# Optimization experiments

Measured on AMD Instinct MI355X. Metric: run time of the kernel, lower is better.

## Reference

```python
import jax, jax.numpy as jnp
import numpy as np
import math
from jax import lax

D = 256      # d_model = out_channel
NH = 8       # n_heads
DEP = D // NH
DFF = 1024
B = 48       # conv batch == attended axis in this model
CIN = 32
HW = 32
S = 30 * 30  # (HW-2)**2 after 3x3 valid conv
OUT = 1
FMAX = float(np.finfo(np.float32).max)


def _p(k, shp, scale=0.02):
    return jax.random.normal(k, shp, jnp.float32) * scale


def setup_inputs():
    key = jax.random.key(0)
    ks = jax.random.split(key, 34)
    return {
        'X_en': jax.random.normal(ks[0], (B, CIN, HW, HW), jnp.float32),
        'X_de': jax.random.normal(ks[1], (B, CIN, HW, HW), jnp.float32),
        'conv1_w': _p(ks[2], (D, CIN, 3, 3)), 'conv1_b': _p(ks[3], (D,)),
        'conv2_w': _p(ks[4], (D, D, 3, 3)), 'conv2_b': _p(ks[5], (D,)),
        'enc_wq': _p(ks[6], (D, D)), 'enc_wk': _p(ks[7], (D, D)), 'enc_wv': _p(ks[8], (D, D)),
        'enc_rel_w': _p(ks[9], (S, NH, DEP, B)),
        'enc_ffn_w1': _p(ks[10], (DFF, D)), 'enc_ffn_b1': _p(ks[11], (DFF,)),
        'enc_ffn_w2': _p(ks[12], (D, DFF)), 'enc_ffn_b2': _p(ks[13], (D,)),
        'dec_m_wq': _p(ks[14], (D, D)), 'dec_m_wk': _p(ks[15], (D, D)), 'dec_m_wv': _p(ks[16], (D, D)),
        'dec_m_rel_w': _p(ks[17], (S, NH, DEP, B)),
        'dec_m_lin1_w': _p(ks[18], (B, B)), 'dec_m_lin1_b': _p(ks[19], (B,)),
        'dec_m_lin2_w': _p(ks[20], (B, B)), 'dec_m_lin2_b': _p(ks[21], (B,)),
        'dec_c_wq': _p(ks[22], (D, D)), 'dec_c_wk': _p(ks[23], (D, D)), 'dec_c_wv': _p(ks[24], (D, D)),
        'dec_c_rel_w': _p(ks[25], (S, NH, DEP, B)),
        'dec_ffn_w1': _p(ks[26], (DFF, D)), 'dec_ffn_b1': _p(ks[27], (DFF,)),
        'dec_ffn_w2': _p(ks[28], (D, DFF)), 'dec_ffn_b2': _p(ks[29], (D,)),
        'out_w': _p(ks[30], (OUT, D)), 'out_b': _p(ks[31], (OUT,)),
    }


def _ln(x, eps=1e-5):
    m = jnp.mean(x, -1, keepdims=True)
    v = jnp.mean((x - m) ** 2, -1, keepdims=True)
    return (x - m) / jnp.sqrt(v + eps)


def _skew(q, w):
    # Music-Transformer relative-position skew: matmul + pad + reshape + slice
    emd = jnp.einsum('shbd,shdj->shbj', q, w)  # (S,NH,b,b)
    s, h, i, j = emd.shape
    l = i + j - 1
    x = jnp.concatenate([emd, jnp.zeros_like(emd)], -1).reshape(s, h, -1)
    pad = (-x.shape[-1]) % l
    x = jnp.pad(x, ((0, 0), (0, 0), (0, pad)))
    return x.reshape(s, h, -1, l)[:, :, :i, i - 1:]


def _mha(xq, xk, xv, wq, wk, wv, rel_w, lins=None):
    b, sl, d = xq.shape
    # raw view (not transpose): (b,sl,d) -> (sl,b,NH,DEP), then swap to (sl,NH,b,DEP)
    q = (xq @ wq.T).reshape(sl, b, NH, DEP).swapaxes(1, 2)
    k = (xk @ wk.T).reshape(sl, b, NH, DEP).swapaxes(1, 2)
    v = (xv @ wv.T).reshape(sl, b, NH, DEP).swapaxes(1, 2)
    scores = jnp.einsum('shid,shjd->shij', q, k) / math.sqrt(DEP)  # (sl,NH,b,b)
    if lins is not None:  # masked path: per-call linears + causal mask
        l1w, l1b, l2w, l2b = lins
        qk = scores @ l1w.T + l1b
        qk = jnp.swapaxes(qk, 2, 3) @ l2w.T + l2b
        mask = jnp.triu(jnp.full((b, b), -FMAX, jnp.float32), 1)
        bmm = qk + mask
    else:
        bmm = scores  # linear1/linear2 outputs are discarded when mask=False
    attn = jax.nn.softmax(bmm + _skew(q, rel_w), axis=0)  # softmax over dim 0 (S)
    out = jnp.einsum('shij,shjd->shid', attn, v)  # (sl,NH,b,DEP)
    return out.reshape(b, sl, NH * DEP)  # view(a_s[2], a_s[0], -1)


def reference(X_en, X_de, conv1_w, conv1_b, conv2_w, conv2_b, enc_wq, enc_wk, enc_wv, enc_rel_w, enc_ffn_w1, enc_ffn_b1, enc_ffn_w2, enc_ffn_b2, dec_m_wq, dec_m_wk, dec_m_wv, dec_m_rel_w, dec_m_lin1_w, dec_m_lin1_b, dec_m_lin2_w, dec_m_lin2_b, dec_c_wq, dec_c_wk, dec_c_wv, dec_c_rel_w, dec_ffn_w1, dec_ffn_b1, dec_ffn_w2, dec_ffn_b2, out_w, out_b):
    def conv(x, w, b_, pad):
        y = lax.conv_general_dilated(x, w, (1, 1), [(pad, pad), (pad, pad)],
                                     dimension_numbers=('NCHW', 'OIHW', 'NCHW'))
        return y + b_[None, :, None, None]

    def convs(x):
        return conv(conv(x, conv1_w, conv1_b, 0), conv2_w, conv2_b, 1)

    xpe = convs(X_en)
    xpd = convs(X_de)
    b, d, h, w = xpe.shape
    x_en = xpe.reshape(b, h * w, d)  # raw reshape as in torch source
    x_de = xpd.reshape(b, h * w, d)
    # encoder layer
    a = _mha(x_en, x_en, x_en, enc_wq, enc_wk, enc_wv, enc_rel_w)
    o1 = _ln(x_en + a)
    f = jax.nn.relu(o1 @ enc_ffn_w1.T + enc_ffn_b1) @ enc_ffn_w2.T + enc_ffn_b2
    enc_out = _ln(o1 + f)
    # decoder layer
    m = _mha(x_de, x_de, x_de, dec_m_wq, dec_m_wk, dec_m_wv, dec_m_rel_w,
             (dec_m_lin1_w, dec_m_lin1_b, dec_m_lin2_w, dec_m_lin2_b))
    h1 = _ln(x_de + m)
    c = _mha(h1, enc_out, enc_out, dec_c_wq, dec_c_wk, dec_c_wv, dec_c_rel_w)
    h2 = _ln(c + h1)
    f2 = jax.nn.relu(h2 @ dec_ffn_w1.T + dec_ffn_b1) @ dec_ffn_w2.T + dec_ffn_b2
    h3 = _ln(h2 + f2)
    y = h3 @ out_w.T + out_b
    return jax.nn.softmax(y, axis=0)
```

## Files before the change

### kernel.cpp

```cpp
#include <hip/hip_runtime.h>
#include <float.h>

typedef __bf16 bf16;
typedef __attribute__((ext_vector_type(8))) __bf16 bf16x8;
typedef __attribute__((ext_vector_type(4))) __bf16 bf16x4;
typedef __attribute__((ext_vector_type(4))) float f32x4;

__device__ __forceinline__ int imin(int a, int b) { return a < b ? a : b; }

__device__ __forceinline__ void gl2lds(const bf16* g, bf16* l) {
  __builtin_amdgcn_global_load_lds(
      (const __attribute__((address_space(1))) void*)g,
      (__attribute__((address_space(3))) void*)l, 16, 0, 0);
}

__global__ void k_zero(bf16* zp) { zp[threadIdx.x] = (bf16)0.0f; }

struct CastSegs { const float* s[13]; bf16* d[13]; int n[13]; };
__global__ void k_cast_all(CastSegs sg, int total) {
  int i = blockIdx.x * 256 + threadIdx.x;
  if (i >= total) return;
  for (int k = 0; k < 13; ++k) {
    if (i < sg.n[k]) { sg.d[k][i] = (bf16)sg.s[k][i]; return; }
    i -= sg.n[k];
  }
}

__global__ __launch_bounds__(256) void k_prep_rel(const float* __restrict__ rel,
                                                  bf16* __restrict__ RelT) {
  __shared__ float tile[32 * 49];
  const int t = threadIdx.x;
  for (int u = 0; u < 8; ++u) {
    const size_t sh = (size_t)blockIdx.x * 8 + u;
    const float* src = rel + sh * 1536;
    bf16* dst = RelT + sh * 1536;
    __syncthreads();
    for (int i = t; i < 1536; i += 256) {
      int k = i / 48, j = i - k * 48;
      tile[k * 49 + j] = src[i];
    }
    __syncthreads();
    for (int i = t; i < 1536; i += 256) {
      int j = i >> 5, k = i & 31;
      dst[i] = (bf16)tile[k * 49 + j];
    }
  }
}

__global__ void k_prep_lin(const float* __restrict__ l1w, const float* __restrict__ l2w,
                           bf16* __restrict__ L1p, bf16* __restrict__ L2p) {
  for (int i = threadIdx.x; i < 3456; i += 256) {
    int r = i / 72, c = i - r * 72;
    L1p[i] = (c < 48) ? (bf16)l1w[r * 48 + c] : (bf16)0.0f;
    L2p[i] = (c < 48) ? (bf16)l2w[r * 48 + c] : (bf16)0.0f;
  }
}

__global__ void k_prep_x(const float* __restrict__ X, bf16* __restrict__ XR) {
  int idx = blockIdx.x * 256 + threadIdx.x;
  if (idx >= 48 * 1024 * 32) return;
  int b = idx >> 15, r = idx & 32767, pos = r >> 5, ic = r & 31;
  XR[idx] = (bf16)X[((size_t)(b * 32 + ic) << 10) + pos];
}

__global__ void k_pack_conv(const float* __restrict__ w, bf16* __restrict__ dst,
                            int OC, int IC, int total) {
  int idx = blockIdx.x * 256 + threadIdx.x;
  if (idx >= total) return;
  int t = idx / (OC * IC);
  int rem = idx - t * OC * IC;
  int oc = rem / IC, ic = rem - oc * IC;
  dst[idx] = (bf16)w[(size_t)(oc * IC + ic) * 9 + t];
}

__global__ __launch_bounds__(256, 2) void k_gemm128(
    const bf16* __restrict__ A, const bf16* __restrict__ B,
    const float* __restrict__ bias, bf16* __restrict__ C,
    int M, int N, int K, int relu, int ldc, int coff) {
  __shared__ alignas(16) bf16 SM[8192];
  bf16* As = SM;
  bf16* Bs = SM + 4096;
  const int t = threadIdx.x, wave = t >> 6;
  const int lane = t & 63, fr = lane & 15, kq = lane >> 4;
  const int wm = wave & 1, wn = wave >> 1;
  const int m0 = blockIdx.x * 128, n0 = blockIdx.y * 128;
  const int srow = t >> 2, kseg = (t & 3) * 8;
  f32x4 acc[4][4] = {};
  const bf16* gA0 = A + (size_t)imin(m0 + srow, M - 1) * K + kseg;
  const bf16* gA1 = A + (size_t)imin(m0 + 64 + srow, M - 1) * K + kseg;
  const bf16* gB0 = B + (size_t)(n0 + srow) * K + kseg;
  const bf16* gB1 = B + (size_t)(n0 + 64 + srow) * K + kseg;
  bf16* sA0 = As + wave * 512;
  bf16* sA1 = As + 2048 + wave * 512;
  bf16* sB0 = Bs + wave * 512;
  bf16* sB1 = Bs + 2048 + wave * 512;
  for (int k0 = 0; k0 < K; k0 += 32) {
    gl2lds(gA0 + k0, sA0);
    gl2lds(gA1 + k0, sA1);
    gl2lds(gB0 + k0, sB0);
    gl2lds(gB1 + k0, sB1);
    __syncthreads();
    bf16x8 af[4], bw[4];
    for (int mt = 0; mt < 4; ++mt)
      af[mt] = *(const bf16x8*)(As + (wm * 64 + mt * 16 + fr) * 32 + kq * 8);
    for (int nt = 0; nt < 4; ++nt)
      bw[nt] = *(const bf16x8*)(Bs + (wn * 64 + nt * 16 + fr) * 32 + kq * 8);
    for (int mt = 0; mt < 4; ++mt)
      for (int nt = 0; nt < 4; ++nt)
        acc[mt][nt] = __builtin_amdgcn_mfma_f32_16x16x32_bf16(af[mt], bw[nt], acc[mt][nt], 0, 0, 0);
    __syncthreads();
  }
  bf16* Cst = SM;
  for (int half = 0; half < 2; ++half) {
    if (wm == half) {
      for (int mt = 0; mt < 4; ++mt)
        for (int nt = 0; nt < 4; ++nt) {
          int n = n0 + wn * 64 + nt * 16 + fr;
          float bv = bias ? bias[n] : 0.0f;
          for (int r = 0; r < 4; ++r) {
            float v = acc[mt][nt][r] + bv;
            if (relu) v = fmaxf(v, 0.0f);
            Cst[(mt * 16 + kq * 4 + r) * 128 + wn * 64 + nt * 16 + fr] = (bf16)v;
          }
        }
    }
    __syncthreads();
    for (int i = t; i < 1024; i += 256) {
      int r = i >> 4, cs = i & 15;
      int gm = m0 + half * 64 + r;
      if (gm < M)
        *(bf16x8*)(C + (size_t)gm * ldc + coff + n0 + cs * 8) = *(const bf16x8*)(Cst + r * 128 + cs * 8);
    }
    __syncthreads();
  }
}

template <int CIN, int PAD, int SRCW, int SRCROWS, int CHECK, int TRANS>
__global__ __launch_bounds__(256, 2) void k_conv128(
    const bf16* __restrict__ A, const bf16* __restrict__ Bp,
    const float* __restrict__ bias, bf16* __restrict__ C,
    const bf16* __restrict__ zpage) {
  __shared__ alignas(16) bf16 SM[8192];
  bf16* As = SM;
  bf16* Bs = SM + 4096;
  const int t = threadIdx.x, wave = t >> 6;
  const int lane = t & 63, fr = lane & 15, kq = lane >> 4;
  const int wm = wave & 1, wn = wave >> 1;
  const int m0 = blockIdx.x * 128, n0 = blockIdx.y * 128;
  const int srow = t >> 2, kseg = (t & 3) * 8;
  f32x4 acc[4][4] = {};
  int bb[2], yy[2], xx[2];
  for (int hf = 0; hf < 2; ++hf) {
    int m = imin(m0 + hf * 64 + srow, 43199);
    int b = m / 900, p = m - b * 900;
    bb[hf] = b; yy[hf] = p / 30; xx[hf] = p - (p / 30) * 30;
  }
  bf16* sA0 = As + wave * 512;
  bf16* sA1 = As + 2048 + wave * 512;
  bf16* sB0 = Bs + wave * 512;
  bf16* sB1 = Bs + 2048 + wave * 512;
  for (int k0 = 0; k0 < CIN; k0 += 32) {
    for (int t9 = 0; t9 < 9; ++t9) {
      const int ky = t9 / 3, kx = t9 - ky * 3;
      const bf16* ga[2];
      for (int hf = 0; hf < 2; ++hf) {
        int sy = yy[hf] + ky - PAD, sx = xx[hf] + kx - PAD;
        bool valid = !CHECK || (sy >= 0 && sy < SRCW && sx >= 0 && sx < SRCW);
        ga[hf] = (valid ? A + (size_t)(bb[hf] * SRCROWS + sy * SRCW + sx) * CIN : zpage) + kseg;
      }
      const bf16* gb = Bp + (size_t)(t9 * 256 + n0 + srow) * CIN + kseg;
      gl2lds(ga[0] + k0, sA0);
      gl2lds(ga[1] + k0, sA1);
      gl2lds(gb + k0, sB0);
      gl2lds(gb + (size_t)64 * CIN + k0, sB1);
      __syncthreads();
      bf16x8 af[4], bw[4];
      for (int mt = 0; mt < 4; ++mt)
        af[mt] = *(const bf16x8*)(As + (wm * 64 + mt * 16 + fr) * 32 + kq * 8);
      for (int nt = 0; nt < 4; ++nt)
        bw[nt] = *(const bf16x8*)(Bs + (wn * 64 + nt * 16 + fr) * 32 + kq * 8);
      for (int mt = 0; mt < 4; ++mt)
        for (int nt = 0; nt < 4; ++nt)
          acc[mt][nt] = __builtin_amdgcn_mfma_f32_16x16x32_bf16(af[mt], bw[nt], acc[mt][nt], 0, 0, 0);
      __syncthreads();
    }
  }
  bf16* Cst = SM;
  for (int half = 0; half < 2; ++half) {
    if (wm == half) {
      for (int mt = 0; mt < 4; ++mt)
        for (int nt = 0; nt < 4; ++nt) {
          int n = n0 + wn * 64 + nt * 16 + fr;
          float bv = bias[n];
          for (int r = 0; r < 4; ++r) {
            float v = acc[mt][nt][r] + bv;
            if (TRANS)
              Cst[(wn * 64 + nt * 16 + fr) * 64 + mt * 16 + kq * 4 + r] = (bf16)v;
            else
              Cst[(mt * 16 + kq * 4 + r) * 128 + wn * 64 + nt * 16 + fr] = (bf16)v;
          }
        }
    }
    __syncthreads();
    if (TRANS) {
      for (int i = t; i < 2048; i += 256) {
        int oc = i >> 4, pc = i & 15;
        int gm = m0 + half * 64 + pc * 4;
        if (gm < 43200) {
          int b = gm / 900, p = gm - b * 900;
          *(bf16x4*)(C + (size_t)(b * 256 + n0 + oc) * 900 + p) = *(const bf16x4*)(Cst + oc * 64 + pc * 4);
        }
      }
    } else {
      for (int i = t; i < 1024; i += 256) {
        int r = i >> 4, cs = i & 15;
        int gm = m0 + half * 64 + r;
        if (gm < 43200)
          *(bf16x8*)(C + (size_t)gm * 256 + n0 + cs * 8) = *(const bf16x8*)(Cst + r * 128 + cs * 8);
      }
    }
    __syncthreads();
  }
}

template <int MASKED>
__global__ __launch_bounds__(256, MASKED ? 4 : 5) void k_attn_z(
    const bf16* __restrict__ QKV, const bf16* __restrict__ RelT, bf16* __restrict__ Z,
    const bf16* __restrict__ L1p, const bf16* __restrict__ L2p,
    const float* __restrict__ l1b, const float* __restrict__ l2b) {
  __shared__ alignas(16) bf16 QKs[2][48 * 40];
  __shared__ float EMD[48 * 49];
  __shared__ alignas(16) bf16 zst[48 * 48];
  __shared__ alignas(16) bf16 Sc[MASKED ? 48 * 72 : 8];
  __shared__ alignas(16) bf16 T2b[MASKED ? 48 * 72 : 8];
  const int sh = blockIdx.x, s = sh >> 3, h = sh & 7;
  const int t = threadIdx.x, wave = t >> 6, lane = t & 63, fr = lane & 15, kq = lane >> 4;
  const float scale = 0.17677669529663687f;
  for (int c = t; c < 384; c += 256) {
    int half = c >= 192 ? 1 : 0, cc = c - half * 192;
    int row = cc >> 2, seg = cc & 3;
    *(bf16x8*)(&QKs[half][row * 40 + seg * 8]) =
        *(const bf16x8*)(QKV + (size_t)(s * 48 + row) * 768 + half * 256 + h * 32 + seg * 8);
  }
  if constexpr (MASKED) {
    for (int i = t; i < 768; i += 256) {
      int r = i >> 4, c = 48 + (i & 15);
      Sc[r * 72 + c] = (bf16)0.0f;
      T2b[r * 72 + c] = (bf16)0.0f;
    }
  }
  __syncthreads();
  const bf16* relb = RelT + (size_t)sh * 1536;
  f32x4 sreg[3];
  int u = 0;
  for (int t9 = wave; t9 < 9; t9 += 4, ++u) {
    int ti = t9 / 3, tj = t9 - ti * 3;
    bf16x8 af = *(const bf16x8*)(&QKs[0][(ti * 16 + fr) * 40 + kq * 8]);
    bf16x8 bk = *(const bf16x8*)(&QKs[1][(tj * 16 + fr) * 40 + kq * 8]);
    bf16x8 rf = *(const bf16x8*)(relb + (tj * 16 + fr) * 32 + kq * 8);
    f32x4 sacc = {}, eacc = {};
    sacc = __builtin_amdgcn_mfma_f32_16x16x32_bf16(af, bk, sacc, 0, 0, 0);
    eacc = __builtin_amdgcn_mfma_f32_16x16x32_bf16(af, rf, eacc, 0, 0, 0);
    for (int r = 0; r < 4; ++r)
      EMD[(ti * 16 + kq * 4 + r) * 49 + tj * 16 + fr] = eacc[r];
    if constexpr (MASKED) {
      for (int r = 0; r < 4; ++r)
        Sc[(ti * 16 + kq * 4 + r) * 72 + tj * 16 + fr] = (bf16)(sacc[r] * scale);
    } else {
      for (int r = 0; r < 4; ++r) sreg[u][r] = sacc[r] * scale;
    }
  }
  __syncthreads();
  if constexpr (!MASKED) {
    u = 0;
    for (int t9 = wave; t9 < 9; t9 += 4, ++u) {
      int ti = t9 / 3, tj = t9 - ti * 3;
      for (int r = 0; r < 4; ++r) {
        int i = ti * 16 + kq * 4 + r, j = tj * 16 + fr;
        float v = sreg[u][r];
        if (j <= i) v += EMD[i * 49 + 47 + j - i];
        zst[i * 48 + j] = (bf16)v;
      }
    }
  } else {
    for (int t9 = wave; t9 < 9; t9 += 4) {
      int ti = t9 / 3, tj = t9 - ti * 3;
      f32x4 a2 = {};
      for (int k0 = 0; k0 < 64; k0 += 32) {
        bf16x8 af = *(const bf16x8*)(Sc + (ti * 16 + fr) * 72 + k0 + kq * 8);
        bf16x8 bw = *(const bf16x8*)(L1p + (tj * 16 + fr) * 72 + k0 + kq * 8);
        a2 = __builtin_amdgcn_mfma_f32_16x16x32_bf16(af, bw, a2, 0, 0, 0);
      }
      for (int r = 0; r < 4; ++r) {
        int i = ti * 16 + kq * 4 + r, a = tj * 16 + fr;
        T2b[a * 72 + i] = (bf16)(a2[r] + l1b[a]);
      }
    }
    __syncthreads();
    for (int t9 = wave; t9 < 9; t9 += 4) {
      int ti = t9 / 3, tj = t9 - ti * 3;
      f32x4 a2 = {};
      for (int k0 = 0; k0 < 64; k0 += 32) {
        bf16x8 af = *(const bf16x8*)(T2b + (ti * 16 + fr) * 72 + k0 + kq * 8);
        bf16x8 bw = *(const bf16x8*)(L2p + (tj * 16 + fr) * 72 + k0 + kq * 8);
        a2 = __builtin_amdgcn_mfma_f32_16x16x32_bf16(af, bw, a2, 0, 0, 0);
      }
      for (int r = 0; r < 4; ++r) {
        int aa = ti * 16 + kq * 4 + r, cc = tj * 16 + fr;
        float v;
        if (cc > aa) v = -10000.0f;
        else v = a2[r] + l2b[cc] + EMD[aa * 49 + 47 + cc - aa];
        zst[aa * 48 + cc] = (bf16)v;
      }
    }
  }
  __syncthreads();
  bf16* zb = Z + (size_t)sh * 2304;
  for (int c = t; c < 288; c += 256)
    *(bf16x8*)(zb + c * 8) = *(const bf16x8*)(zst + c * 8);
}

__global__ __launch_bounds__(256) void k_colstats(const bf16* __restrict__ Z,
                                                  float* __restrict__ Mc, float* __restrict__ Ic) {
  __shared__ float rm[16][136], rs[16][136];
  const int t = threadIdx.x, cg = t & 15, sg = t >> 4;
  const bf16* p = Z + blockIdx.x * 128 + cg * 8;
  const int s0 = sg * 57, s1 = imin(900, s0 + 57);
  float m[8], ss[8];
  for (int e = 0; e < 8; ++e) { m[e] = -FLT_MAX; ss[e] = 0.0f; }
  for (int s = s0; s < s1; ++s) {
    bf16x8 zv = *(const bf16x8*)(p + (size_t)s * 18432);
    for (int e = 0; e < 8; ++e) {
      float v = (float)zv[e];
      if (v > m[e]) { ss[e] *= __expf(m[e] - v); m[e] = v; }
      ss[e] += __expf(v - m[e]);
    }
  }
  for (int e = 0; e < 8; ++e) { rm[sg][cg * 8 + e] = m[e]; rs[sg][cg * 8 + e] = ss[e]; }
  __syncthreads();
  if (t < 128) {
    float M2 = -FLT_MAX;
    for (int g = 0; g < 16; ++g) M2 = fmaxf(M2, rm[g][t]);
    float S2 = 0.0f;
    for (int g = 0; g < 16; ++g) S2 += rs[g][t] * __expf(rm[g][t] - M2);
    Mc[blockIdx.x * 128 + t] = M2;
    Ic[blockIdx.x * 128 + t] = 1.0f / S2;
  }
}

__global__ __launch_bounds__(256, 6) void k_attn_av(
    const bf16* __restrict__ Z, const bf16* __restrict__ QKV,
    const float* __restrict__ Mc, const float* __restrict__ Ic, bf16* __restrict__ O) {
  __shared__ alignas(16) bf16 Ps[48 * 72];
  __shared__ alignas(16) bf16 Vt[32 * 72];
  __shared__ alignas(16) bf16 Ost[48 * 32];
  const int sh = blockIdx.x, s = sh >> 3, h = sh & 7;
  const int t = threadIdx.x, wave = t >> 6, lane = t & 63, fr = lane & 15, kq = lane >> 4;
  for (int i = t; i < 768; i += 256) Ps[(i >> 4) * 72 + 48 + (i & 15)] = (bf16)0.0f;
  for (int i = t; i < 512; i += 256) Vt[(i >> 4) * 72 + 48 + (i & 15)] = (bf16)0.0f;
  const bf16* zb = Z + (size_t)sh * 2304;
  const float* mc = Mc + h * 2304;
  const float* ic = Ic + h * 2304;
  for (int c = t; c < 288; c += 256) {
    int r = c / 6, seg = c - r * 6;
    int idx = r * 48 + seg * 8;
    bf16x8 zv = *(const bf16x8*)(zb + idx);
    f32x4 m0v = *(const f32x4*)(mc + idx), m1v = *(const f32x4*)(mc + idx + 4);
    f32x4 i0v = *(const f32x4*)(ic + idx), i1v = *(const f32x4*)(ic + idx + 4);
    bf16x8 pv;
    for (int e = 0; e < 4; ++e) pv[e] = (bf16)(__expf((float)zv[e] - m0v[e]) * i0v[e]);
    for (int e = 0; e < 4; ++e) pv[4 + e] = (bf16)(__expf((float)zv[4 + e] - m1v[e]) * i1v[e]);
    *(bf16x8*)(Ps + r * 72 + seg * 8) = pv;
  }
  for (int c = t; c < 192; c += 256) {
    int j = c >> 2, seg = c & 3;
    bf16x8 v = *(const bf16x8*)(QKV + (size_t)(s * 48 + j) * 768 + 512 + h * 32 + seg * 8);
    for (int e = 0; e < 8; ++e) Vt[(seg * 8 + e) * 72 + j] = v[e];
  }
  __syncthreads();
  for (int t6 = wave; t6 < 6; t6 += 4) {
    int ti = t6 >> 1, td = t6 & 1;
    f32x4 a2 = {};
    for (int k0 = 0; k0 < 64; k0 += 32) {
      bf16x8 af = *(const bf16x8*)(Ps + (ti * 16 + fr) * 72 + k0 + kq * 8);
      bf16x8 bv = *(const bf16x8*)(Vt + (td * 16 + fr) * 72 + k0 + kq * 8);
      a2 = __builtin_amdgcn_mfma_f32_16x16x32_bf16(af, bv, a2, 0, 0, 0);
    }
    for (int r = 0; r < 4; ++r)
      Ost[(ti * 16 + kq * 4 + r) * 32 + td * 16 + fr] = (bf16)a2[r];
  }
  __syncthreads();
  bf16* ob = O + (size_t)sh * 1536;
  for (int c = t; c < 192; c += 256)
    *(bf16x8*)(ob + c * 8) = *(const bf16x8*)(Ost + c * 8);
}

__global__ __launch_bounds__(256) void k_add_ln(
    const bf16* __restrict__ Xa, const bf16* __restrict__ Xb, bf16* __restrict__ out) {
  const int t = threadIdx.x, lane = t & 63, w = t >> 6;
  const size_t off = ((size_t)blockIdx.x * 4 + w) * 256 + lane * 4;
  bf16x4 av = *(const bf16x4*)(Xa + off);
  bf16x4 bv = *(const bf16x4*)(Xb + off);
  f32x4 x;
  for (int c = 0; c < 4; ++c) x[c] = (float)av[c] + (float)bv[c];
  float sum = x[0] + x[1] + x[2] + x[3];
  for (int o = 1; o < 64; o <<= 1) sum += __shfl_xor(sum, o);
  float mean = sum * (1.0f / 256.0f);
  float q = 0.0f;
  for (int c = 0; c < 4; ++c) { float d = x[c] - mean; q += d * d; }
  for (int o = 1; o < 64; o <<= 1) q += __shfl_xor(q, o);
  float rstd = rsqrtf(q * (1.0f / 256.0f) + 1e-5f);
  bf16x4 y;
  for (int c = 0; c < 4; ++c) y[c] = (bf16)((x[c] - mean) * rstd);
  *(bf16x4*)(out + off) = y;
}

__global__ __launch_bounds__(256) void k_ydot(
    const bf16* __restrict__ H, const float* __restrict__ w,
    const float* __restrict__ b, float* __restrict__ Y) {
  const int t = threadIdx.x, lane = t & 63, wv = t >> 6;
  const size_t row = (size_t)blockIdx.x * 4 + wv;
  bf16x4 hx = *(const bf16x4*)(H + row * 256 + lane * 4);
  f32x4 ww = *(const f32x4*)(w + lane * 4);
  float s = (float)hx[0] * ww[0] + (float)hx[1] * ww[1] + (float)hx[2] * ww[2] + (float)hx[3] * ww[3];
  for (int o = 1; o < 64; o <<= 1) s += __shfl_xor(s, o);
  if (lane == 0) Y[row] = s + b[0];
}

__global__ void k_softmax48(const float* __restrict__ Y, float* __restrict__ O) {
  int ss = blockIdx.x * 256 + threadIdx.x;
  if (ss >= 900) return;
  float m = -FLT_MAX;
  for (int b = 0; b < 48; ++b) m = fmaxf(m, Y[b * 900 + ss]);
  float sum = 0.0f;
  for (int b = 0; b < 48; ++b) sum += __expf(Y[b * 900 + ss] - m);
  float inv = 1.0f / sum;
  for (int b = 0; b < 48; ++b) O[b * 900 + ss] = __expf(Y[b * 900 + ss] - m) * inv;
}

extern "C" void kernel_launch(void* const* d_in, const int* in_sizes, int n_in,
                              void* d_out, int out_size, void* d_ws, size_t ws_size,
                              hipStream_t stream) {
  (void)in_sizes; (void)n_in; (void)out_size;
  const float* X_en = (const float*)d_in[0];
  const float* X_de = (const float*)d_in[1];
  const float* conv1_w = (const float*)d_in[2];
  const float* conv1_b = (const float*)d_in[3];
  const float* conv2_w = (const float*)d_in[4];
  const float* conv2_b = (const float*)d_in[5];
  const float* enc_wq = (const float*)d_in[6];
  const float* enc_wk = (const float*)d_in[7];
  const float* enc_wv = (const float*)d_in[8];
  const float* enc_rel = (const float*)d_in[9];
  const float* enc_f1w = (const float*)d_in[10];
  const float* enc_f1b = (const float*)d_in[11];
  const float* enc_f2w = (const float*)d_in[12];
  const float* enc_f2b = (const float*)d_in[13];
  const float* dm_wq = (const float*)d_in[14];
  const float* dm_wk = (const float*)d_in[15];
  const float* dm_wv = (const float*)d_in[16];
  const float* dm_rel = (const float*)d_in[17];
  const float* dm_l1w = (const float*)d_in[18];
  const float* dm_l1b = (const float*)d_in[19];
  const float* dm_l2w = (const float*)d_in[20];
  const float* dm_l2b = (const float*)d_in[21];
  const float* dc_wq = (const float*)d_in[22];
  const float* dc_wk = (const float*)d_in[23];
  const float* dc_wv = (const float*)d_in[24];
  const float* dc_rel = (const float*)d_in[25];
  const float* d_f1w = (const float*)d_in[26];
  const float* d_f1b = (const float*)d_in[27];
  const float* d_f2w = (const float*)d_in[28];
  const float* d_f2b = (const float*)d_in[29];
  const float* out_w = (const float*)d_in[30];
  const float* out_b = (const float*)d_in[31];
  float* OUT = (float*)d_out;

  const size_t SLOT = 22118400;
  char* ws = (char*)d_ws;
  size_t o = 0;
  bf16* S1 = (bf16*)(ws + o); o += SLOT;
  bf16* S2 = (bf16*)(ws + o); o += SLOT;
  bf16* S3 = (bf16*)(ws + o); o += SLOT;
  bf16* S4 = (bf16*)(ws + o); o += SLOT;
  bf16* S5 = (bf16*)(ws + o); o += SLOT;
  char* U = ws + o; o += 33177600 + 3 * SLOT;
  bf16* Zb = (bf16*)U;
  bf16* QKV = (bf16*)(U + 33177600);
  bf16* XR = (bf16*)U;
  bf16* C1R = (bf16*)(U + 3145728);
  bf16* HID = (bf16*)U;
  bf16* wa = (bf16*)(ws + o); o += 4603904 + 16384;
  float* Y = (float*)(ws + o); o += 172800;
  if (ws_size < o) return;

  bf16* zpage = (bf16*)Y;
  float* encM = (float*)S4; float* encI = encM + 18432;
  float* dmM  = (float*)S3; float* dmI  = dmM + 18432;
  float* crM  = (float*)S2; float* crI  = crM + 18432;
  bf16* encRel = S3;
  bf16* dmRel  = S5;
  bf16* crRel  = S3;

  bf16* c1p = wa;
  bf16* c2p = wa + 73728;
  bf16* EQKVw = wa + 663552;
  bf16* MQKVw = wa + 860160;
  bf16* cqw = wa + 1056768;
  bf16* CKVw = wa + 1122304;
  bf16* ef1 = wa + 1253376;
  bf16* ef2 = wa + 1515520;
  bf16* df1 = wa + 1777664;
  bf16* df2 = wa + 2039808;
  bf16* L1p = wa + 2301952;
  bf16* L2p = wa + 2305408;

  auto gemm = [&](const bf16* A, const bf16* B, const float* bias, bf16* C,
                  int M, int N, int K, int relu, int ldc, int coff) {
    k_gemm128<<<dim3((M + 127) / 128, N / 128), dim3(256), 0, stream>>>(
        A, B, bias, C, M, N, K, relu, ldc, coff);
  };

  k_zero<<<dim3(1), dim3(256), 0, stream>>>(zpage);
  k_pack_conv<<<dim3(288), dim3(256), 0, stream>>>(conv1_w, c1p, 256, 32, 73728);
  k_pack_conv<<<dim3(2304), dim3(256), 0, stream>>>(conv2_w, c2p, 256, 256, 589824);
  k_prep_lin<<<dim3(1), dim3(256), 0, stream>>>(dm_l1w, dm_l2w, L1p, L2p);
  {
    CastSegs sg;
    const float* srcs[13] = {enc_wq, enc_wk, enc_wv, dm_wq, dm_wk, dm_wv, dc_wq,
                             dc_wk, dc_wv, enc_f1w, enc_f2w, d_f1w, d_f2w};
    bf16* dsts[13] = {EQKVw, EQKVw + 65536, EQKVw + 131072, MQKVw, MQKVw + 65536,
                      MQKVw + 131072, cqw, CKVw, CKVw + 65536, ef1, ef2, df1, df2};
    int ns[13] = {65536, 65536, 65536, 65536, 65536, 65536, 65536, 65536, 65536,
                  262144, 262144, 262144, 262144};
    int total = 0;
    for (int k = 0; k < 13; ++k) { sg.s[k] = srcs[k]; sg.d[k] = dsts[k]; sg.n[k] = ns[k]; total += ns[k]; }
    k_cast_all<<<dim3((total + 255) / 256), dim3(256), 0, stream>>>(sg, total);
  }

  auto conv_chain = [&](const float* X, bf16* outB) {
    k_prep_x<<<dim3(6144), dim3(256), 0, stream>>>(X, XR);
    k_conv128<32, 0, 32, 1024, 0, 0><<<dim3(338, 2), dim3(256), 0, stream>>>(XR, c1p, conv1_b, C1R, zpage);
    k_conv128<256, 1, 30, 900, 1, 1><<<dim3(338, 2), dim3(256), 0, stream>>>(C1R, c2p, conv2_b, outB, zpage);
  };
  conv_chain(X_en, S1);
  conv_chain(X_de, S2);

  gemm(S1, EQKVw, nullptr, QKV, 43200, 768, 256, 0, 768, 0);
  k_prep_rel<<<dim3(900), dim3(256), 0, stream>>>(enc_rel, encRel);
  k_attn_z<0><<<dim3(7200), dim3(256), 0, stream>>>(QKV, encRel, Zb, nullptr, nullptr, nullptr, nullptr);
  k_colstats<<<dim3(144), dim3(256), 0, stream>>>(Zb, encM, encI);
  k_attn_av<<<dim3(7200), dim3(256), 0, stream>>>(Zb, QKV, encM, encI, S5);
  k_add_ln<<<dim3(10800), dim3(256), 0, stream>>>(S1, S5, S3);
  gemm(S3, ef1, enc_f1b, HID, 43200, 1024, 256, 1, 1024, 0);
  gemm(HID, ef2, enc_f2b, S5, 43200, 256, 1024, 0, 256, 0);
  k_add_ln<<<dim3(10800), dim3(256), 0, stream>>>(S3, S5, S1);

  gemm(S2, MQKVw, nullptr, QKV, 43200, 768, 256, 0, 768, 0);
  k_prep_rel<<<dim3(900), dim3(256), 0, stream>>>(dm_rel, dmRel);
  k_attn_z<1><<<dim3(7200), dim3(256), 0, stream>>>(QKV, dmRel, Zb, L1p, L2p, dm_l1b, dm_l2b);
  k_colstats<<<dim3(144), dim3(256), 0, stream>>>(Zb, dmM, dmI);
  k_attn_av<<<dim3(7200), dim3(256), 0, stream>>>(Zb, QKV, dmM, dmI, S5);
  k_add_ln<<<dim3(10800), dim3(256), 0, stream>>>(S2, S5, S4);

  gemm(S4, cqw, nullptr, QKV, 43200, 256, 256, 0, 768, 0);
  gemm(S1, CKVw, nullptr, QKV, 43200, 512, 256, 0, 768, 256);
  k_prep_rel<<<dim3(900), dim3(256), 0, stream>>>(dc_rel, crRel);
  k_attn_z<0><<<dim3(7200), dim3(256), 0, stream>>>(QKV, crRel, Zb, nullptr, nullptr, nullptr, nullptr);
  k_colstats<<<dim3(144), dim3(256), 0, stream>>>(Zb, crM, crI);
  k_attn_av<<<dim3(7200), dim3(256), 0, stream>>>(Zb, QKV, crM, crI, S5);
  k_add_ln<<<dim3(10800), dim3(256), 0, stream>>>(S5, S4, S3);

  gemm(S3, df1, d_f1b, HID, 43200, 1024, 256, 1, 1024, 0);
  gemm(HID, df2, d_f2b, S5, 43200, 256, 1024, 0, 256, 0);
  k_add_ln<<<dim3(10800), dim3(256), 0, stream>>>(S3, S5, S4);
  k_ydot<<<dim3(10800), dim3(256), 0, stream>>>(S4, out_w, out_b, Y);
  k_softmax48<<<dim3(4), dim3(256), 0, stream>>>(Y, OUT);
}
```

Baseline: 1.105 ms.

## Batch encoder/decoder convs, deepen GEMM K-step, merge cross-attn projections

The encoder and decoder conv chains are merged into single launches over 96 images, and conv2 gets a dedicated kernel that loads 64-wide K chunks per barrier. The generic GEMM now also stages 64 K elements per sync, doubling LDS, and can select between two A/B operand pairs so the cross-attention Q and KV projections run as one launch. Column stats use smaller column groups to launch twice as many blocks, and two tiny prep kernels are fused. These cut launch count and sync overhead, at the cost of more LDS per block, which may lower occupancy, and a larger intermediate buffer.

```diff
diff --git a/kernel.cpp b/kernel.cpp
--- a/kernel.cpp
+++ b/kernel.cpp
@@ -14,7 +14,16 @@
       (__attribute__((address_space(3))) void*)l, 16, 0, 0);
 }
 
-__global__ void k_zero(bf16* zp) { zp[threadIdx.x] = (bf16)0.0f; }
+__global__ void k_prep_misc(bf16* zp, const float* __restrict__ l1w,
+                            const float* __restrict__ l2w,
+                            bf16* __restrict__ L1p, bf16* __restrict__ L2p) {
+  zp[threadIdx.x] = (bf16)0.0f;
+  for (int i = threadIdx.x; i < 3456; i += 256) {
+    int r = i / 72, c = i - r * 72;
+    L1p[i] = (c < 48) ? (bf16)l1w[r * 48 + c] : (bf16)0.0f;
+    L2p[i] = (c < 48) ? (bf16)l2w[r * 48 + c] : (bf16)0.0f;
+  }
+}
 
 struct CastSegs { const float* s[13]; bf16* d[13]; int n[13]; };
 __global__ void k_cast_all(CastSegs sg, int total) {
@@ -47,20 +56,14 @@
   }
 }
 
-__global__ void k_prep_lin(const float* __restrict__ l1w, const float* __restrict__ l2w,
-                           bf16* __restrict__ L1p, bf16* __restrict__ L2p) {
-  for (int i = threadIdx.x; i < 3456; i += 256) {
-    int r = i / 72, c = i - r * 72;
-    L1p[i] = (c < 48) ? (bf16)l1w[r * 48 + c] : (bf16)0.0f;
-    L2p[i] = (c < 48) ? (bf16)l2w[r * 48 + c] : (bf16)0.0f;
-  }
-}
-
-__global__ void k_prep_x(const float* __restrict__ X, bf16* __restrict__ XR) {
+__global__ void k_prep_x(const float* __restrict__ XE, const float* __restrict__ XD,
+                         bf16* __restrict__ XR) {
   int idx = blockIdx.x * 256 + threadIdx.x;
-  if (idx >= 48 * 1024 * 32) return;
+  if (idx >= 96 * 1024 * 32) return;
   int b = idx >> 15, r = idx & 32767, pos = r >> 5, ic = r & 31;
-  XR[idx] = (bf16)X[((size_t)(b * 32 + ic) << 10) + pos];
+  const float* X = (b < 48) ? XE : XD;
+  int bl = (b < 48) ? b : b - 48;
+  XR[idx] = (bf16)X[((size_t)(bl * 32 + ic) << 10) + pos];
 }
 
 __global__ void k_pack_conv(const float* __restrict__ w, bf16* __restrict__ dst,
@@ -74,40 +77,49 @@
 }
 
 __global__ __launch_bounds__(256, 2) void k_gemm128(
-    const bf16* __restrict__ A, const bf16* __restrict__ B,
+    const bf16* __restrict__ A, const bf16* __restrict__ A2,
+    const bf16* __restrict__ B, const bf16* __restrict__ B2, int nsplit,
     const float* __restrict__ bias, bf16* __restrict__ C,
     int M, int N, int K, int relu, int ldc, int coff) {
-  __shared__ alignas(16) bf16 SM[8192];
+  __shared__ alignas(16) bf16 SM[16384];
   bf16* As = SM;
-  bf16* Bs = SM + 4096;
+  bf16* Asx = SM + 4096;
+  bf16* Bs = SM + 8192;
+  bf16* Bsx = SM + 12288;
   const int t = threadIdx.x, wave = t >> 6;
   const int lane = t & 63, fr = lane & 15, kq = lane >> 4;
   const int wm = wave & 1, wn = wave >> 1;
   const int m0 = blockIdx.x * 128, n0 = blockIdx.y * 128;
   const int srow = t >> 2, kseg = (t & 3) * 8;
+  const bf16* Ause = A; const bf16* Buse = B; int nloc = n0;
+  if (n0 >= nsplit) { Ause = A2; Buse = B2; nloc = n0 - nsplit; }
   f32x4 acc[4][4] = {};
-  const bf16* gA0 = A + (size_t)imin(m0 + srow, M - 1) * K + kseg;
-  const bf16* gA1 = A + (size_t)imin(m0 + 64 + srow, M - 1) * K + kseg;
-  const bf16* gB0 = B + (size_t)(n0 + srow) * K + kseg;
-  const bf16* gB1 = B + (size_t)(n0 + 64 + srow) * K + kseg;
+  const bf16* gA0 = Ause + (size_t)imin(m0 + srow, M - 1) * K + kseg;
+  const bf16* gA1 = Ause + (size_t)imin(m0 + 64 + srow, M - 1) * K + kseg;
+  const bf16* gB0 = Buse + (size_t)(nloc + srow) * K + kseg;
+  const bf16* gB1 = Buse + (size_t)(nloc + 64 + srow) * K + kseg;
   bf16* sA0 = As + wave * 512;
   bf16* sA1 = As + 2048 + wave * 512;
   bf16* sB0 = Bs + wave * 512;
   bf16* sB1 = Bs + 2048 + wave * 512;
-  for (int k0 = 0; k0 < K; k0 += 32) {
-    gl2lds(gA0 + k0, sA0);
-    gl2lds(gA1 + k0, sA1);
-    gl2lds(gB0 + k0, sB0);
-    gl2lds(gB1 + k0, sB1);
-    __syncthreads();
-    bf16x8 af[4], bw[4];
-    for (int mt = 0; mt < 4; ++mt)
-      af[mt] = *(const bf16x8*)(As + (wm * 64 + mt * 16 + fr) * 32 + kq * 8);
-    for (int nt = 0; nt < 4; ++nt)
-      bw[nt] = *(const bf16x8*)(Bs + (wn * 64 + nt * 16 + fr) * 32 + kq * 8);
-    for (int mt = 0; mt < 4; ++mt)
+  for (int k0 = 0; k0 < K; k0 += 64) {
+    gl2lds(gA0 + k0, sA0);          gl2lds(gA0 + k0 + 32, sA0 + 4096);
+    gl2lds(gA1 + k0, sA1);          gl2lds(gA1 + k0 + 32, sA1 + 4096);
+    gl2lds(gB0 + k0, sB0);          gl2lds(gB0 + k0 + 32, sB0 + 4096);
+    gl2lds(gB1 + k0, sB1);          gl2lds(gB1 + k0 + 32, sB1 + 4096);
+    __syncthreads();
+    for (int ch = 0; ch < 2; ++ch) {
+      const bf16* Ac = ch ? Asx : As;
+      const bf16* Bc = ch ? Bsx : Bs;
+      bf16x8 af[4], bw[4];
+      for (int mt = 0; mt < 4; ++mt)
+        af[mt] = *(const bf16x8*)(Ac + (wm * 64 + mt * 16 + fr) * 32 + kq * 8);
       for (int nt = 0; nt < 4; ++nt)
-        acc[mt][nt] = __builtin_amdgcn_mfma_f32_16x16x32_bf16(af[mt], bw[nt], acc[mt][nt], 0, 0, 0);
+        bw[nt] = *(const bf16x8*)(Bc + (wn * 64 + nt * 16 + fr) * 32 + kq * 8);
+      for (int mt = 0; mt < 4; ++mt)
+        for (int nt = 0; nt < 4; ++nt)
+          acc[mt][nt] = __builtin_amdgcn_mfma_f32_16x16x32_bf16(af[mt], bw[nt], acc[mt][nt], 0, 0, 0);
+    }
     __syncthreads();
   }
   bf16* Cst = SM;
@@ -135,7 +147,7 @@
   }
 }
 
-template <int CIN, int PAD, int SRCW, int SRCROWS, int CHECK, int TRANS>
+template <int CIN, int PAD, int SRCW, int SRCROWS, int CHECK, int TRANS, int MTOT>
 __global__ __launch_bounds__(256, 2) void k_conv128(
     const bf16* __restrict__ A, const bf16* __restrict__ Bp,
     const float* __restrict__ bias, bf16* __restrict__ C,
@@ -151,7 +163,7 @@
   f32x4 acc[4][4] = {};
   int bb[2], yy[2], xx[2];
   for (int hf = 0; hf < 2; ++hf) {
-    int m = imin(m0 + hf * 64 + srow, 43199);
+    int m = imin(m0 + hf * 64 + srow, MTOT - 1);
     int b = m / 900, p = m - b * 900;
     bb[hf] = b; yy[hf] = p / 30; xx[hf] = p - (p / 30) * 30;
   }
@@ -206,7 +218,7 @@
       for (int i = t; i < 2048; i += 256) {
         int oc = i >> 4, pc = i & 15;
         int gm = m0 + half * 64 + pc * 4;
-        if (gm < 43200) {
+        if (gm < MTOT) {
           int b = gm / 900, p = gm - b * 900;
           *(bf16x4*)(C + (size_t)(b * 256 + n0 + oc) * 900 + p) = *(const bf16x4*)(Cst + oc * 64 + pc * 4);
         }
@@ -215,9 +227,86 @@
       for (int i = t; i < 1024; i += 256) {
         int r = i >> 4, cs = i & 15;
         int gm = m0 + half * 64 + r;
-        if (gm < 43200)
+        if (gm < MTOT)
           *(bf16x8*)(C + (size_t)gm * 256 + n0 + cs * 8) = *(const bf16x8*)(Cst + r * 128 + cs * 8);
       }
+    }
+    __syncthreads();
+  }
+}
+
+__global__ __launch_bounds__(256, 2) void k_conv2x(
+    const bf16* __restrict__ A, const bf16* __restrict__ Bp,
+    const float* __restrict__ bias, bf16* __restrict__ C,
+    const bf16* __restrict__ zpage) {
+  __shared__ alignas(16) bf16 SM[16384];
+  bf16* As = SM;
+  bf16* Bs = SM + 8192;
+  const int t = threadIdx.x, wave = t >> 6;
+  const int lane = t & 63, fr = lane & 15, kq = lane >> 4;
+  const int wm = wave & 1, wn = wave >> 1;
+  const int m0 = blockIdx.x * 128, n0 = blockIdx.y * 128;
+  const int srow = t >> 2, kseg = (t & 3) * 8;
+  f32x4 acc[4][4] = {};
+  int bb[2], yy[2], xx[2];
+  for (int hf = 0; hf < 2; ++hf) {
+    int m = imin(m0 + hf * 64 + srow, 86399);
+    int b = m / 900, p = m - b * 900;
+    bb[hf] = b; yy[hf] = p / 30; xx[hf] = p - (p / 30) * 30;
+  }
+  bf16* sA0 = As + wave * 512;
+  bf16* sA1 = As + 2048 + wave * 512;
+  bf16* sB0 = Bs + wave * 512;
+  bf16* sB1 = Bs + 2048 + wave * 512;
+  for (int k0 = 0; k0 < 256; k0 += 64) {
+    for (int t9 = 0; t9 < 9; ++t9) {
+      const int ky = t9 / 3, kx = t9 - ky * 3;
+      const bf16* ga[2];
+      for (int hf = 0; hf < 2; ++hf) {
+        int sy = yy[hf] + ky - 1, sx = xx[hf] + kx - 1;
+        bool valid = (sy >= 0 && sy < 30 && sx >= 0 && sx < 30);
+        ga[hf] = (valid ? A + (size_t)(bb[hf] * 900 + sy * 30 + sx) * 256 : zpage) + kseg;
+      }
+      const bf16* gb = Bp + (size_t)(t9 * 256 + n0 + srow) * 256 + kseg;
+      gl2lds(ga[0] + k0, sA0);               gl2lds(ga[0] + k0 + 32, sA0 + 4096);
+      gl2lds(ga[1] + k0, sA1);               gl2lds(ga[1] + k0 + 32, sA1 + 4096);
+      gl2lds(gb + k0, sB0);                  gl2lds(gb + k0 + 32, sB0 + 4096);
+      gl2lds(gb + 64 * 256 + k0, sB1);       gl2lds(gb + 64 * 256 + k0 + 32, sB1 + 4096);
+      __syncthreads();
+      for (int ch = 0; ch < 2; ++ch) {
+        const bf16* Ac = As + ch * 4096;
+        const bf16* Bc = Bs + ch * 4096;
+        bf16x8 af[4], bw[4];
+        for (int mt = 0; mt < 4; ++mt)
+          af[mt] = *(const bf16x8*)(Ac + (wm * 64 + mt * 16 + fr) * 32 + kq * 8);
+        for (int nt = 0; nt < 4; ++nt)
+          bw[nt] = *(const bf16x8*)(Bc + (wn * 64 + nt * 16 + fr) * 32 + kq * 8);
+        for (int mt = 0; mt < 4; ++mt)
+          for (int nt = 0; nt < 4; ++nt)
+            acc[mt][nt] = __builtin_amdgcn_mfma_f32_16x16x32_bf16(af[mt], bw[nt], acc[mt][nt], 0, 0, 0);
+      }
+      __syncthreads();
+    }
+  }
+  bf16* Cst = SM;
+  for (int half = 0; half < 2; ++half) {
+    if (wm == half) {
+      for (int mt = 0; mt < 4; ++mt)
+        for (int nt = 0; nt < 4; ++nt) {
+          int n = n0 + wn * 64 + nt * 16 + fr;
+          float bv = bias[n];
+          for (int r = 0; r < 4; ++r) {
+            float v = acc[mt][nt][r] + bv;
+            Cst[(wn * 64 + nt * 16 + fr) * 64 + mt * 16 + kq * 4 + r] = (bf16)v;
+          }
+        }
+    }
+    __syncthreads();
+    for (int i = t; i < 2048; i += 256) {
+      int oc = i >> 4, pc = i & 15;
+      int gm = m0 + half * 64 + pc * 4;
+      int b = gm / 900, p = gm - b * 900;
+      *(bf16x4*)(C + (size_t)(b * 256 + n0 + oc) * 900 + p) = *(const bf16x4*)(Cst + oc * 64 + pc * 4);
     }
     __syncthreads();
   }
@@ -322,10 +411,10 @@
 
 __global__ __launch_bounds__(256) void k_colstats(const bf16* __restrict__ Z,
                                                   float* __restrict__ Mc, float* __restrict__ Ic) {
-  __shared__ float rm[16][136], rs[16][136];
-  const int t = threadIdx.x, cg = t & 15, sg = t >> 4;
-  const bf16* p = Z + blockIdx.x * 128 + cg * 8;
-  const int s0 = sg * 57, s1 = imin(900, s0 + 57);
+  __shared__ float rm[32][72], rs[32][72];
+  const int t = threadIdx.x, cg = t & 7, sg = t >> 3;
+  const bf16* p = Z + blockIdx.x * 64 + cg * 8;
+  const int s0 = sg * 29, s1 = imin(900, s0 + 29);
   float m[8], ss[8];
   for (int e = 0; e < 8; ++e) { m[e] = -FLT_MAX; ss[e] = 0.0f; }
   for (int s = s0; s < s1; ++s) {
@@ -338,13 +427,13 @@
   }
   for (int e = 0; e < 8; ++e) { rm[sg][cg * 8 + e] = m[e]; rs[sg][cg * 8 + e] = ss[e]; }
   __syncthreads();
-  if (t < 128) {
+  if (t < 64) {
     float M2 = -FLT_MAX;
-    for (int g = 0; g < 16; ++g) M2 = fmaxf(M2, rm[g][t]);
+    for (int g = 0; g < 32; ++g) M2 = fmaxf(M2, rm[g][t]);
     float S2 = 0.0f;
-    for (int g = 0; g < 16; ++g) S2 += rs[g][t] * __expf(rm[g][t] - M2);
-    Mc[blockIdx.x * 128 + t] = M2;
-    Ic[blockIdx.x * 128 + t] = 1.0f / S2;
+    for (int g = 0; g < 32; ++g) S2 += rs[g][t] * __expf(rm[g][t] - M2);
+    Mc[blockIdx.x * 64 + t] = M2;
+    Ic[blockIdx.x * 64 + t] = 1.0f / S2;
   }
 }
 
@@ -488,7 +577,7 @@
   bf16* Zb = (bf16*)U;
   bf16* QKV = (bf16*)(U + 33177600);
   bf16* XR = (bf16*)U;
-  bf16* C1R = (bf16*)(U + 3145728);
+  bf16* C1R = (bf16*)(U + 12582912);
   bf16* HID = (bf16*)U;
   bf16* wa = (bf16*)(ws + o); o += 4603904 + 16384;
   float* Y = (float*)(ws + o); o += 172800;
@@ -518,13 +607,12 @@
   auto gemm = [&](const bf16* A, const bf16* B, const float* bias, bf16* C,
                   int M, int N, int K, int relu, int ldc, int coff) {
     k_gemm128<<<dim3((M + 127) / 128, N / 128), dim3(256), 0, stream>>>(
-        A, B, bias, C, M, N, K, relu, ldc, coff);
+        A, A, B, B, N, bias, C, M, N, K, relu, ldc, coff);
   };
 
-  k_zero<<<dim3(1), dim3(256), 0, stream>>>(zpage);
+  k_prep_misc<<<dim3(1), dim3(256), 0, stream>>>(zpage, dm_l1w, dm_l2w, L1p, L2p);
   k_pack_conv<<<dim3(288), dim3(256), 0, stream>>>(conv1_w, c1p, 256, 32, 73728);
   k_pack_conv<<<dim3(2304), dim3(256), 0, stream>>>(conv2_w, c2p, 256, 256, 589824);
-  k_prep_lin<<<dim3(1), dim3(256), 0, stream>>>(dm_l1w, dm_l2w, L1p, L2p);
   {
     CastSegs sg;
     const float* srcs[13] = {enc_wq, enc_wk, enc_wv, dm_wq, dm_wk, dm_wv, dc_wq,
@@ -538,18 +626,15 @@
     k_cast_all<<<dim3((total + 255) / 256), dim3(256), 0, stream>>>(sg, total);
   }
 
-  auto conv_chain = [&](const float* X, bf16* outB) {
-    k_prep_x<<<dim3(6144), dim3(256), 0, stream>>>(X, XR);
-    k_conv128<32, 0, 32, 1024, 0, 0><<<dim3(338, 2), dim3(256), 0, stream>>>(XR, c1p, conv1_b, C1R, zpage);
-    k_conv128<256, 1, 30, 900, 1, 1><<<dim3(338, 2), dim3(256), 0, stream>>>(C1R, c2p, conv2_b, outB, zpage);
-  };
-  conv_chain(X_en, S1);
-  conv_chain(X_de, S2);
+  k_prep_x<<<dim3(12288), dim3(256), 0, stream>>>(X_en, X_de, XR);
+  k_conv128<32, 0, 32, 1024, 0, 0, 86400><<<dim3(675, 2), dim3(256), 0, stream>>>(
+      XR, c1p, conv1_b, C1R, zpage);
+  k_conv2x<<<dim3(675, 2), dim3(256), 0, stream>>>(C1R, c2p, conv2_b, S1, zpage);
 
   gemm(S1, EQKVw, nullptr, QKV, 43200, 768, 256, 0, 768, 0);
   k_prep_rel<<<dim3(900), dim3(256), 0, stream>>>(enc_rel, encRel);
   k_attn_z<0><<<dim3(7200), dim3(256), 0, stream>>>(QKV, encRel, Zb, nullptr, nullptr, nullptr, nullptr);
-  k_colstats<<<dim3(144), dim3(256), 0, stream>>>(Zb, encM, encI);
+  k_colstats<<<dim3(288), dim3(256), 0, stream>>>(Zb, encM, encI);
   k_attn_av<<<dim3(7200), dim3(256), 0, stream>>>(Zb, QKV, encM, encI, S5);
   k_add_ln<<<dim3(10800), dim3(256), 0, stream>>>(S1, S5, S3);
   gemm(S3, ef1, enc_f1b, HID, 43200, 1024, 256, 1, 1024, 0);
@@ -559,15 +644,15 @@
   gemm(S2, MQKVw, nullptr, QKV, 43200, 768, 256, 0, 768, 0);
   k_prep_rel<<<dim3(900), dim3(256), 0, stream>>>(dm_rel, dmRel);
   k_attn_z<1><<<dim3(7200), dim3(256), 0, stream>>>(QKV, dmRel, Zb, L1p, L2p, dm_l1b, dm_l2b);
-  k_colstats<<<dim3(144), dim3(256), 0, stream>>>(Zb, dmM, dmI);
+  k_colstats<<<dim3(288), dim3(256), 0, stream>>>(Zb, dmM, dmI);
   k_attn_av<<<dim3(7200), dim3(256), 0, stream>>>(Zb, QKV, dmM, dmI, S5);
   k_add_ln<<<dim3(10800), dim3(256), 0, stream>>>(S2, S5, S4);
 
-  gemm(S4, cqw, nullptr, QKV, 43200, 256, 256, 0, 768, 0);
-  gemm(S1, CKVw, nullptr, QKV, 43200, 512, 256, 0, 768, 256);
+  k_gemm128<<<dim3(338, 6), dim3(256), 0, stream>>>(
+      S4, S1, cqw, CKVw, 256, nullptr, QKV, 43200, 768, 256, 0, 768, 0);
   k_prep_rel<<<dim3(900), dim3(256), 0, stream>>>(dc_rel, crRel);
   k_attn_z<0><<<dim3(7200), dim3(256), 0, stream>>>(QKV, crRel, Zb, nullptr, nullptr, nullptr, nullptr);
-  k_colstats<<<dim3(144), dim3(256), 0, stream>>>(Zb, crM, crI);
+  k_colstats<<<dim3(288), dim3(256), 0, stream>>>(Zb, crM, crI);
   k_attn_av<<<dim3(7200), dim3(256), 0, stream>>>(Zb, QKV, crM, crI, S5);
   k_add_ln<<<dim3(10800), dim3(256), 0, stream>>>(S5, S4, S3);
 
```

After: 1.026 ms. -7.1%, faster.
